# Kernel optimization log

Hardware: AMD Instinct MI355X
Metric: run time of the kernel (lower is better)

Reference implementation:

```python
import jax, jax.numpy as jnp
import numpy as np

B, L, DM, H, DFF = 4, 2048, 512, 8, 2048
D = DM // H            # head dim = 64
FACTOR = 5
U = min(FACTOR * int(np.ceil(np.log(L))), L)  # 40 sampled keys / top-u queries
EPS = 1e-5


def layer_norm(x, g, b):
    m = x.mean(-1, keepdims=True)
    v = ((x - m) ** 2).mean(-1, keepdims=True)
    return (x - m) * jax.lax.rsqrt(v + EPS) * g + b


def setup_inputs() -> dict:
    key = jax.random.key(0)
    ks = jax.random.split(key, 18)
    s = 0.02  # init scale for stability
    return {
        "x": jax.random.normal(ks[0], (B, L, DM), jnp.float32),
        "Wq": jax.random.normal(ks[1], (DM, DM), jnp.float32) * s,
        "bq": jnp.zeros((DM,), jnp.float32),
        "Wk": jax.random.normal(ks[2], (DM, DM), jnp.float32) * s,
        "bk": jnp.zeros((DM,), jnp.float32),
        "Wv": jax.random.normal(ks[3], (DM, DM), jnp.float32) * s,
        "bv": jnp.zeros((DM,), jnp.float32),
        "Wo": jax.random.normal(ks[4], (DM, DM), jnp.float32) * s,
        "bo": jnp.zeros((DM,), jnp.float32),
        "Wc1": jax.random.normal(ks[5], (DFF, DM), jnp.float32) * s,  # conv1d k=1 weight (out,in)
        "bc1": jnp.zeros((DFF,), jnp.float32),
        "Wc2": jax.random.normal(ks[6], (DM, DFF), jnp.float32) * s,
        "bc2": jnp.zeros((DM,), jnp.float32),
        "ln1_g": jnp.ones((DM,), jnp.float32),
        "ln1_b": jnp.zeros((DM,), jnp.float32),
        "ln2_g": jnp.ones((DM,), jnp.float32),
        "ln2_b": jnp.zeros((DM,), jnp.float32),
        "sample_idx": jax.random.randint(ks[7], (L, U), 0, L, jnp.int32),
    }


def reference(x, Wq, bq, Wk, bk, Wv, bv, Wo, bo, Wc1, bc1, Wc2, bc2,
              ln1_g, ln1_b, ln2_g, ln2_b, sample_idx):
    Bb, Ll, _ = x.shape
    # --- AttentionLayer projections -> (B, H, L, D) ---
    q = (x @ Wq + bq).reshape(Bb, Ll, H, D).transpose(0, 2, 1, 3)
    k = (x @ Wk + bk).reshape(Bb, Ll, H, D).transpose(0, 2, 1, 3)
    v = (x @ Wv + bv).reshape(Bb, Ll, H, D).transpose(0, 2, 1, 3)

    # --- ProbSparse: score each query against U sampled keys ---
    K_sample = k[:, :, sample_idx, :]                       # (B,H,L,U,D)
    QK_sample = jnp.einsum('bhld,bhlud->bhlu', q, K_sample)  # (B,H,L,U)
    M = QK_sample.max(-1) - QK_sample.mean(-1)               # sparsity measure (B,H,L)
    _, M_top = jax.lax.top_k(M, U)                           # (B,H,U) top-u query indices

    # --- full attention only for top-u queries ---
    Q_red = jnp.take_along_axis(q, M_top[..., None], axis=2)  # (B,H,U,D)
    scores = jnp.einsum('bhud,bhld->bhul', Q_red, k) / jnp.sqrt(jnp.float32(D))
    attn = jax.nn.softmax(scores, axis=-1)                    # (B,H,U,L)
    ctx_top = jnp.einsum('bhul,bhld->bhud', attn, v)          # (B,H,U,D)

    # --- initial context = mean of V (mask_flag=False); scatter top-u rows ---
    context = jnp.broadcast_to(v.mean(axis=2, keepdims=True), v.shape)
    bi = jnp.arange(Bb)[:, None, None]
    hi = jnp.arange(H)[None, :, None]
    context = context.at[bi, hi, M_top].set(ctx_top)          # (B,H,L,D)

    new_x = context.transpose(0, 2, 1, 3).reshape(Bb, Ll, DM) @ Wo + bo

    # --- residual + norm + conv1d(k=1) FFN + norm ---
    x = layer_norm(x + new_x, ln1_g, ln1_b)
    y = jax.nn.relu(x @ Wc1.T + bc1)
    y = y @ Wc2.T + bc2
    return layer_norm(x + y, ln2_g, ln2_b)
```

## Files before the change

kernel.cpp:

```cpp
#include <hip/hip_runtime.h>
#include <math.h>

static constexpr int Bc = 4, Lc = 2048, DMc = 512, Hc = 8, Dc = 64, DFFc = 2048, Uc = 40;
static constexpr int NT = Bc * Lc;

typedef __attribute__((ext_vector_type(4))) float f32x4;
typedef __attribute__((ext_vector_type(8))) short bf16x8;
typedef unsigned short ushort_t;

__device__ __forceinline__ float wave_sum(float v) {
#pragma unroll
  for (int off = 32; off > 0; off >>= 1) v += __shfl_xor(v, off);
  return v;
}

__device__ __forceinline__ ushort_t f2bf(float f) {
  union { float f; unsigned int u; } c{f};
  unsigned int u = c.u + 0x7fff + ((c.u >> 16) & 1);
  return (ushort_t)(u >> 16);
}

__device__ __forceinline__ float bf2f(ushort_t b) {
  union { unsigned int u; float f; } c{(unsigned int)b << 16};
  return c.f;
}

__device__ __forceinline__ void gload16(const ushort_t* g, ushort_t* l) {
  __builtin_amdgcn_global_load_lds(
      (const __attribute__((address_space(1))) unsigned int*)g,
      (__attribute__((address_space(3))) unsigned int*)l, 16, 0, 0);
}

template <int MODE>
__global__ __launch_bounds__(256) void gemm_mfma(
    const ushort_t* __restrict__ A, const ushort_t* __restrict__ Bt,
    const float* __restrict__ bias, float* __restrict__ Cf,
    ushort_t* __restrict__ Cb, ushort_t* __restrict__ Qo, ushort_t* __restrict__ Ko,
    ushort_t* __restrict__ Vo, int M, int N, int K) {
  __shared__ __align__(16) ushort_t As[128 * 32];
  __shared__ __align__(16) ushort_t Bs[128 * 32];
  const int tid = threadIdx.x;
  const int lane = tid & 63, wave = tid >> 6;
  const int nwg = gridDim.x * gridDim.y;
  const int lin = blockIdx.y * gridDim.x + blockIdx.x;
  const int swz = (lin & 7) * (nwg >> 3) + (lin >> 3);
  const int m0 = (swz / gridDim.x) << 7, n0 = (swz % gridDim.x) << 7;
  const int wm = ((wave >> 1) << 6), wn = ((wave & 1) << 6);
  f32x4 acc[4][4] = {};
  const ushort_t* aSrc = A + (size_t)(m0 + (tid >> 2)) * K + ((tid & 3) << 3);
  const ushort_t* bSrc = Bt + (size_t)(n0 + (tid >> 2)) * K + ((tid & 3) << 3);
  ushort_t* aDst = As + wave * 512;
  ushort_t* bDst = Bs + wave * 512;
  const size_t aHalf = (size_t)64 * K, bHalf = (size_t)64 * K;
  for (int k0 = 0; k0 < K; k0 += 32) {
    gload16(aSrc + k0, aDst);
    gload16(aSrc + aHalf + k0, aDst + 2048);
    gload16(bSrc + k0, bDst);
    gload16(bSrc + bHalf + k0, bDst + 2048);
    __syncthreads();
    bf16x8 af[4], bfr[4];
    const int fr = lane & 15, ko = (lane >> 4) << 3;
#pragma unroll
    for (int i = 0; i < 4; ++i) {
      af[i] = *reinterpret_cast<const bf16x8*>(&As[(wm + i * 16 + fr) * 32 + ko]);
      bfr[i] = *reinterpret_cast<const bf16x8*>(&Bs[(wn + i * 16 + fr) * 32 + ko]);
    }
#pragma unroll
    for (int i = 0; i < 4; ++i)
#pragma unroll
      for (int j = 0; j < 4; ++j)
        acc[i][j] = __builtin_amdgcn_mfma_f32_16x16x32_bf16(af[i], bfr[j], acc[i][j], 0, 0, 0);
    __syncthreads();
  }
  const int cr = (lane >> 4) << 2, cc = lane & 15;
#pragma unroll
  for (int j = 0; j < 4; ++j) {
    const int col = n0 + wn + j * 16 + cc;
    const float bsv = bias[col];
#pragma unroll
    for (int i = 0; i < 4; ++i) {
#pragma unroll
      for (int r = 0; r < 4; ++r) {
        const int row = m0 + wm + i * 16 + cr + r;
        float v = acc[i][j][r] + bsv;
        if (MODE == 0) {
          Cf[(size_t)row * N + col] = v;
        } else if (MODE == 1) {
          Cb[(size_t)row * N + col] = f2bf(fmaxf(v, 0.f));
        } else {
          const int which = col >> 9, h = (col >> 6) & 7, d = col & 63;
          const int b = row >> 11, l = row & (Lc - 1);
          const size_t o = ((size_t)(((b << 3) + h) << 11) + l) * 64 + d;
          ushort_t* dst = which == 0 ? Qo : (which == 1 ? Ko : Vo);
          dst[o] = f2bf(v);
        }
      }
    }
  }
}

__global__ __launch_bounds__(256) void conv_bf16(const float* __restrict__ in,
                                                 ushort_t* __restrict__ out) {
  int i = blockIdx.x * 256 + threadIdx.x;
  float4 v = *reinterpret_cast<const float4*>(&in[(size_t)i * 4]);
  ushort4 o;
  o.x = f2bf(v.x); o.y = f2bf(v.y); o.z = f2bf(v.z); o.w = f2bf(v.w);
  *reinterpret_cast<ushort4*>(&out[(size_t)i * 4]) = o;
}

__global__ __launch_bounds__(256) void tconv(const float* __restrict__ in,
                                             ushort_t* __restrict__ out,
                                             int R, int C, int rowOff) {
  __shared__ float t[32][33];
  const int r0 = blockIdx.y << 5, c0 = blockIdx.x << 5;
  const int tr = threadIdx.x >> 5, tc = threadIdx.x & 31;
#pragma unroll
  for (int p = 0; p < 4; ++p)
    t[tr + p * 8][tc] = in[(size_t)(r0 + tr + p * 8) * C + c0 + tc];
  __syncthreads();
#pragma unroll
  for (int p = 0; p < 4; ++p)
    out[(size_t)(rowOff + c0 + tr + p * 8) * R + r0 + tc] = f2bf(t[tc][tr + p * 8]);
}

__global__ __launch_bounds__(256) void concat_bias(const float* __restrict__ bq,
                                                   const float* __restrict__ bk,
                                                   const float* __restrict__ bv,
                                                   float* __restrict__ o) {
  int i = blockIdx.x * 256 + threadIdx.x;
  o[i] = i < 512 ? bq[i] : (i < 1024 ? bk[i - 512] : bv[i - 1024]);
}

__global__ __launch_bounds__(256) void compute_M_kernel(
    const ushort_t* __restrict__ Q, const ushort_t* __restrict__ K,
    const int* __restrict__ sidx, float* __restrict__ Mout) {
  const int tid = threadIdx.x;
  const int wave = tid >> 6, lane = tid & 63;
  const int g = lane >> 4, lg = lane & 15;
  const int p = blockIdx.x;
  const int xcd = p & 7, j = p >> 3;
  const int bh = xcd + ((j >> 7) << 3);
  const int inner = j & 127;
  const int gw = (bh << 11) + (inner << 4) + wave * 4 + g;
  const int l = gw & (Lc - 1);
  const ushort4 q4 = *reinterpret_cast<const ushort4*>(&Q[((size_t)gw << 6) + (lg << 2)]);
  const float qx = bf2f(q4.x), qy = bf2f(q4.y), qz = bf2f(q4.z), qw = bf2f(q4.w);
  const ushort_t* Kbase = K + ((size_t)bh << 17);
  const int* sp = sidx + l * Uc;
  float mx = -1e30f, sm = 0.f;
#pragma unroll 4
  for (int u = 0; u < Uc; ++u) {
    const int idx = sp[u];
    const ushort4 k4 = *reinterpret_cast<const ushort4*>(&Kbase[((size_t)idx << 6) + (lg << 2)]);
    float d = qx * bf2f(k4.x) + qy * bf2f(k4.y) + qz * bf2f(k4.z) + qw * bf2f(k4.w);
#pragma unroll
    for (int off = 8; off > 0; off >>= 1) d += __shfl_xor(d, off);
    mx = fmaxf(mx, d);
    sm += d;
  }
  if (lg == 0) Mout[gw] = mx - sm * (1.f / Uc);
}

__global__ __launch_bounds__(256) void topk_kernel(const float* __restrict__ Min,
                                                   int* __restrict__ Mtop) {
  __shared__ float sm[Lc];
  const int bh = blockIdx.x >> 3, chunk = blockIdx.x & 7;
  const int tid = threadIdx.x;
  for (int i = tid; i < Lc; i += 256) sm[i] = Min[bh * Lc + i];
  __syncthreads();
  const int cand = (chunk << 8) + tid;
  const float mv = sm[cand];
  int rank = 0;
  for (int j = 0; j < Lc; j += 4) {
    float4 w4 = *reinterpret_cast<const float4*>(&sm[j]);
    rank += (w4.x > mv || (w4.x == mv && (j + 0) < cand));
    rank += (w4.y > mv || (w4.y == mv && (j + 1) < cand));
    rank += (w4.z > mv || (w4.z == mv && (j + 2) < cand));
    rank += (w4.w > mv || (w4.w == mv && (j + 3) < cand));
  }
  if (rank < Uc) Mtop[bh * Uc + rank] = cand;
}

__global__ __launch_bounds__(256, 3) void attn_flash(
    const ushort_t* __restrict__ Q, const ushort_t* __restrict__ K,
    const ushort_t* __restrict__ V, const int* __restrict__ Mtop,
    float* __restrict__ m_p, float* __restrict__ l_p, float* __restrict__ o_p) {
  __shared__ __align__(16) ushort_t Qs[48 * 80];
  __shared__ __align__(16) ushort_t KVs[128 * 80];
  __shared__ __align__(16) ushort_t Ps[48 * 144];
  __shared__ float mw[4][48];
  __shared__ float lw[4][48];
  const int tid = threadIdx.x;
  const int lane = tid & 63, w = tid >> 6;
  const int cc = lane & 15, hi = lane >> 4;
  const int bh = blockIdx.x >> 4, chunk = blockIdx.x & 15;
  const int kk0 = chunk << 7;
  const ushort_t* Qb = Q + ((size_t)bh << 17);
  const ushort_t* Kb = K + ((size_t)bh << 17);
  const ushort_t* Vb = V + ((size_t)bh << 17);

  for (int i = tid; i < 48 * 8; i += 256) {
    const int r = i >> 3, c8 = (i & 7) << 3;
    bf16x8 v = 0;
    if (r < Uc) {
      const int lsel = Mtop[bh * Uc + r];
      v = *reinterpret_cast<const bf16x8*>(&Qb[((size_t)lsel << 6) + c8]);
    }
    *reinterpret_cast<bf16x8*>(&Qs[r * 80 + c8]) = v;
  }
  for (int i = tid; i < 128 * 8; i += 256) {
    const int r = i >> 3, c8 = (i & 7) << 3;
    *reinterpret_cast<bf16x8*>(&KVs[r * 80 + c8]) =
        *reinterpret_cast<const bf16x8*>(&Kb[((size_t)(kk0 + r) << 6) + c8]);
  }
  __syncthreads();

  f32x4 sacc[3][2] = {};
#pragma unroll
  for (int s = 0; s < 2; ++s) {
    bf16x8 af[3], bk[2];
#pragma unroll
    for (int i = 0; i < 3; ++i)
      af[i] = *reinterpret_cast<const bf16x8*>(&Qs[(i * 16 + cc) * 80 + s * 32 + hi * 8]);
#pragma unroll
    for (int jj = 0; jj < 2; ++jj)
      bk[jj] = *reinterpret_cast<const bf16x8*>(&KVs[(w * 32 + jj * 16 + cc) * 80 + s * 32 + hi * 8]);
#pragma unroll
    for (int i = 0; i < 3; ++i)
#pragma unroll
      for (int jj = 0; jj < 2; ++jj)
        sacc[i][jj] = __builtin_amdgcn_mfma_f32_16x16x32_bf16(af[i], bk[jj], sacc[i][jj], 0, 0, 0);
  }

  float mx[3][4];
#pragma unroll
  for (int i = 0; i < 3; ++i)
#pragma unroll
    for (int r = 0; r < 4; ++r)
      mx[i][r] = fmaxf(sacc[i][0][r], sacc[i][1][r]) * 0.125f;
#pragma unroll
  for (int off = 1; off < 16; off <<= 1)
#pragma unroll
    for (int i = 0; i < 3; ++i)
#pragma unroll
      for (int r = 0; r < 4; ++r)
        mx[i][r] = fmaxf(mx[i][r], __shfl_xor(mx[i][r], off));
  if (cc == 0)
#pragma unroll
    for (int i = 0; i < 3; ++i)
#pragma unroll
      for (int r = 0; r < 4; ++r) mw[w][i * 16 + (hi << 2) + r] = mx[i][r];
  __syncthreads();

  float fm[3][4], ls[3][4];
#pragma unroll
  for (int i = 0; i < 3; ++i)
#pragma unroll
    for (int r = 0; r < 4; ++r) {
      const int row = i * 16 + (hi << 2) + r;
      fm[i][r] = fmaxf(fmaxf(mw[0][row], mw[1][row]), fmaxf(mw[2][row], mw[3][row]));
      ls[i][r] = 0.f;
    }
#pragma unroll
  for (int i = 0; i < 3; ++i)
#pragma unroll
    for (int jj = 0; jj < 2; ++jj)
#pragma unroll
      for (int r = 0; r < 4; ++r) {
        float p = __expf(sacc[i][jj][r] * 0.125f - fm[i][r]);
        ls[i][r] += p;
        Ps[(i * 16 + (hi << 2) + r) * 144 + w * 32 + jj * 16 + cc] = f2bf(p);
      }
#pragma unroll
  for (int off = 1; off < 16; off <<= 1)
#pragma unroll
    for (int i = 0; i < 3; ++i)
#pragma unroll
      for (int r = 0; r < 4; ++r) ls[i][r] += __shfl_xor(ls[i][r], off);
  if (cc == 0)
#pragma unroll
    for (int i = 0; i < 3; ++i)
#pragma unroll
      for (int r = 0; r < 4; ++r) lw[w][i * 16 + (hi << 2) + r] = ls[i][r];

  {
    ushort_t* Vt = KVs;
    for (int i = tid; i < 128 * 8; i += 256) {
      const int k = i >> 3, c8 = (i & 7) << 3;
      bf16x8 v = *reinterpret_cast<const bf16x8*>(&Vb[((size_t)(kk0 + k) << 6) + c8]);
#pragma unroll
      for (int jq = 0; jq < 8; ++jq) Vt[(c8 + jq) * 144 + k] = (ushort_t)v[jq];
    }
  }
  __syncthreads();

  f32x4 oacc[3] = {};
#pragma unroll
  for (int s = 0; s < 4; ++s) {
    bf16x8 ap[3], bv;
#pragma unroll
    for (int i = 0; i < 3; ++i)
      ap[i] = *reinterpret_cast<const bf16x8*>(&Ps[(i * 16 + cc) * 144 + s * 32 + hi * 8]);
    bv = *reinterpret_cast<const bf16x8*>(&KVs[(w * 16 + cc) * 144 + s * 32 + hi * 8]);
#pragma unroll
    for (int i = 0; i < 3; ++i)
      oacc[i] = __builtin_amdgcn_mfma_f32_16x16x32_bf16(ap[i], bv, oacc[i], 0, 0, 0);
  }
#pragma unroll
  for (int i = 0; i < 3; ++i)
#pragma unroll
    for (int r = 0; r < 4; ++r) {
      const int row = i * 16 + (hi << 2) + r;
      if (row < Uc)
        o_p[((size_t)((bh * Uc + row) * 16 + chunk) << 6) + w * 16 + cc] = oacc[i][r];
    }
  if (w == 0 && cc == 0)
#pragma unroll
    for (int i = 0; i < 3; ++i)
#pragma unroll
      for (int r = 0; r < 4; ++r) {
        const int row = i * 16 + (hi << 2) + r;
        if (row < Uc) {
          m_p[(bh * Uc + row) * 16 + chunk] = fm[i][r];
          l_p[(bh * Uc + row) * 16 + chunk] =
              lw[0][row] + lw[1][row] + lw[2][row] + lw[3][row];
        }
      }
}

__global__ __launch_bounds__(256) void attn_combine(
    const float* __restrict__ m_p, const float* __restrict__ l_p,
    const float* __restrict__ o_p, const int* __restrict__ Mtop,
    ushort_t* __restrict__ ctxb) {
  const int w = (blockIdx.x * 256 + threadIdx.x) >> 6;
  const int lane = threadIdx.x & 63;
  const float* mp = m_p + w * 16;
  const float* lp = l_p + w * 16;
  float M = -1e30f;
#pragma unroll
  for (int c = 0; c < 16; ++c) M = fmaxf(M, mp[c]);
  float denom = 0.f;
  float wgt[16];
#pragma unroll
  for (int c = 0; c < 16; ++c) {
    wgt[c] = __expf(mp[c] - M);
    denom += lp[c] * wgt[c];
  }
  float acc = 0.f;
#pragma unroll
  for (int c = 0; c < 16; ++c)
    acc += o_p[((size_t)w * 16 + c) * 64 + lane] * wgt[c];
  const int bh = w / Uc;
  const int b = bh >> 3, h = bh & 7;
  const int lsel = Mtop[w];
  ctxb[(size_t)(b * Lc + lsel) * DMc + (h << 6) + lane] = f2bf(acc / denom);
}

__global__ __launch_bounds__(64) void vmean_kernel(const ushort_t* __restrict__ V,
                                                   float* __restrict__ vmean) {
  int blk = blockIdx.x;
  int bh = blk >> 3, c = blk & 7;
  int lane = threadIdx.x;
  float sm = 0.f;
  int lbase = c << 8;
  for (int l = lbase; l < lbase + 256; ++l)
    sm += bf2f(V[((size_t)(bh * Lc + l) << 6) + lane]);
  atomicAdd(&vmean[(bh << 6) + lane], sm * (1.f / Lc));
}

__global__ __launch_bounds__(256) void build_ctx_kernel(const float* __restrict__ vmean,
                                                        ushort_t* __restrict__ ctxb) {
  int idx = blockIdx.x * 256 + threadIdx.x;
  ctxb[idx] = f2bf(vmean[((idx >> 20) << 9) + (idx & 511)]);
}

__global__ __launch_bounds__(256) void add_ln_kernel(
    const float* __restrict__ resid, const float* __restrict__ yin,
    const float* __restrict__ g, const float* __restrict__ bbias,
    float* __restrict__ out, ushort_t* __restrict__ outb) {
  __shared__ float vals[DMc];
  __shared__ float red[4];
  int row = blockIdx.x, tid = threadIdx.x;
  size_t base = (size_t)row * DMc;
  float lsum = 0.f;
  for (int c = tid; c < DMc; c += 256) {
    float t = resid[base + c] + yin[base + c];
    vals[c] = t;
    lsum += t;
  }
  lsum = wave_sum(lsum);
  if ((tid & 63) == 0) red[tid >> 6] = lsum;
  __syncthreads();
  float mean = (red[0] + red[1] + red[2] + red[3]) * (1.f / DMc);
  __syncthreads();
  float lv = 0.f;
  for (int c = tid; c < DMc; c += 256) {
    float dv = vals[c] - mean;
    lv += dv * dv;
  }
  lv = wave_sum(lv);
  if ((tid & 63) == 0) red[tid >> 6] = lv;
  __syncthreads();
  float inv = rsqrtf((red[0] + red[1] + red[2] + red[3]) * (1.f / DMc) + 1e-5f);
  for (int c = tid; c < DMc; c += 256) {
    float o = (vals[c] - mean) * inv * g[c] + bbias[c];
    out[base + c] = o;
    if (outb) outb[base + c] = f2bf(o);
  }
}

extern "C" void kernel_launch(void* const* d_in, const int* in_sizes, int n_in,
                              void* d_out, int out_size, void* d_ws, size_t ws_size,
                              hipStream_t stream) {
  (void)in_sizes; (void)n_in; (void)out_size; (void)ws_size;
  const float* x   = (const float*)d_in[0];
  const float* Wq  = (const float*)d_in[1];
  const float* bq  = (const float*)d_in[2];
  const float* Wk  = (const float*)d_in[3];
  const float* bk  = (const float*)d_in[4];
  const float* Wv  = (const float*)d_in[5];
  const float* bv  = (const float*)d_in[6];
  const float* Wo  = (const float*)d_in[7];
  const float* bo  = (const float*)d_in[8];
  const float* Wc1 = (const float*)d_in[9];
  const float* bc1 = (const float*)d_in[10];
  const float* Wc2 = (const float*)d_in[11];
  const float* bc2 = (const float*)d_in[12];
  const float* g1  = (const float*)d_in[13];
  const float* b1  = (const float*)d_in[14];
  const float* g2  = (const float*)d_in[15];
  const float* b2  = (const float*)d_in[16];
  const int* sidx  = (const int*)d_in[17];
  float* out = (float*)d_out;

  float* ws = (float*)d_ws;
  ushort_t* Qb   = (ushort_t*)ws;
  ushort_t* Kb   = (ushort_t*)(ws + 4194304);
  ushort_t* Vb   = (ushort_t*)(ws + 8388608);
  float* m_p    = ws + 12582912;
  float* l_p    = ws + 12603392;
  float* o_p    = ws + 12623872;
  float* X1     = ws + 16777216;
  ushort_t* xb   = (ushort_t*)(ws + 20971520);
  ushort_t* Wqkvt= (ushort_t*)(ws + 23068672);
  ushort_t* Wot  = (ushort_t*)(ws + 23461888);
  ushort_t* Wc1b = (ushort_t*)(ws + 23592960);
  ushort_t* Wc2b = (ushort_t*)(ws + 24117248);
  float* bqkv   = ws + 24641536;
  float* Mb     = ws + 24643072;
  float* vmean  = ws + 24708608;
  int* Mtop     = (int*)(ws + 24710656);
  ushort_t* CTXb = Vb;
  ushort_t* X1b  = (ushort_t*)(ws + 12582912);
  ushort_t* Yb   = (ushort_t*)ws;

  dim3 blk(256);
  conv_bf16<<<4096, blk, 0, stream>>>(x, xb);
  tconv<<<dim3(16, 16), blk, 0, stream>>>(Wq, Wqkvt, 512, 512, 0);
  tconv<<<dim3(16, 16), blk, 0, stream>>>(Wk, Wqkvt, 512, 512, 512);
  tconv<<<dim3(16, 16), blk, 0, stream>>>(Wv, Wqkvt, 512, 512, 1024);
  tconv<<<dim3(16, 16), blk, 0, stream>>>(Wo, Wot, 512, 512, 0);
  conv_bf16<<<1024, blk, 0, stream>>>(Wc1, Wc1b);
  conv_bf16<<<1024, blk, 0, stream>>>(Wc2, Wc2b);
  concat_bias<<<6, blk, 0, stream>>>(bq, bk, bv, bqkv);

  gemm_mfma<2><<<dim3(12, 64), blk, 0, stream>>>(xb, Wqkvt, bqkv, nullptr, nullptr,
                                                 Qb, Kb, Vb, NT, 1536, DMc);
  compute_M_kernel<<<4096, blk, 0, stream>>>(Qb, Kb, sidx, Mb);
  topk_kernel<<<256, blk, 0, stream>>>(Mb, Mtop);
  attn_flash<<<512, blk, 0, stream>>>(Qb, Kb, Vb, Mtop, m_p, l_p, o_p);
  hipMemsetAsync(vmean, 0, Bc * Hc * Dc * sizeof(float), stream);
  vmean_kernel<<<Bc * Hc * 8, dim3(64), 0, stream>>>(Vb, vmean);
  build_ctx_kernel<<<16384, blk, 0, stream>>>(vmean, CTXb);
  attn_combine<<<320, blk, 0, stream>>>(m_p, l_p, o_p, Mtop, CTXb);

  gemm_mfma<0><<<dim3(4, 64), blk, 0, stream>>>(CTXb, Wot, bo, out, nullptr,
                                                nullptr, nullptr, nullptr,
                                                NT, DMc, DMc);
  add_ln_kernel<<<NT, blk, 0, stream>>>(x, out, g1, b1, X1, X1b);
  gemm_mfma<1><<<dim3(16, 64), blk, 0, stream>>>(X1b, Wc1b, bc1, nullptr, Yb,
                                                 nullptr, nullptr, nullptr,
                                                 NT, DFFc, DMc);
  gemm_mfma<0><<<dim3(4, 64), blk, 0, stream>>>(Yb, Wc2b, bc2, out, nullptr,
                                                nullptr, nullptr, nullptr,
                                                NT, DMc, DFFc);
  add_ln_kernel<<<NT, blk, 0, stream>>>(X1, out, g2, b2, out, nullptr);
}
```

Baseline: 382.0 us.

## Replace brute-force rank top-k with radix bisection threshold and candidate ranking

The top-k kernel changes from ranking all 2048 queries against every other score to one block per (batch, head). Each block maps floats to order-preserving unsigned keys and bisects over the key range with block-wide counts to find the 40th-largest threshold. Only the candidates at or above that threshold are then ranked exactly, with each wave splitting the comparison across its lanes. This removes the O(L^2) comparison work but adds 32 serial bisection rounds, each with two barriers, and launches only 32 blocks, which leaves most of the GPU idle.

Result: faster. 356.8 us (-6.6%).

```diff
diff --git a/kernel.cpp b/kernel.cpp
--- a/kernel.cpp
+++ b/kernel.cpp
@@ -163,22 +163,64 @@
 
 __global__ __launch_bounds__(256) void topk_kernel(const float* __restrict__ Min,
                                                    int* __restrict__ Mtop) {
-  __shared__ float sm[Lc];
-  const int bh = blockIdx.x >> 3, chunk = blockIdx.x & 7;
+  __shared__ unsigned sm[Lc];
+  __shared__ int scount[4];
+  __shared__ int slist[Lc];
+  __shared__ int snum;
+  const int bh = blockIdx.x;
   const int tid = threadIdx.x;
-  for (int i = tid; i < Lc; i += 256) sm[i] = Min[bh * Lc + i];
-  __syncthreads();
-  const int cand = (chunk << 8) + tid;
-  const float mv = sm[cand];
-  int rank = 0;
-  for (int j = 0; j < Lc; j += 4) {
-    float4 w4 = *reinterpret_cast<const float4*>(&sm[j]);
-    rank += (w4.x > mv || (w4.x == mv && (j + 0) < cand));
-    rank += (w4.y > mv || (w4.y == mv && (j + 1) < cand));
-    rank += (w4.z > mv || (w4.z == mv && (j + 2) < cand));
-    rank += (w4.w > mv || (w4.w == mv && (j + 3) < cand));
-  }
-  if (rank < Uc) Mtop[bh * Uc + rank] = cand;
+  const int wv = tid >> 6, lane = tid & 63;
+  unsigned sv[8];
+#pragma unroll
+  for (int t = 0; t < 8; ++t) {
+    const unsigned u = __float_as_uint(Min[bh * Lc + tid + (t << 8)]);
+    const unsigned s = (u & 0x80000000u) ? ~u : (u | 0x80000000u);
+    sv[t] = s;
+    sm[tid + (t << 8)] = s;
+  }
+  if (tid == 0) snum = 0;
+  __syncthreads();
+  unsigned lo = 0u, hi = 0xFFFFFFFFu;
+  while (lo < hi) {
+    const unsigned mid =
+        (unsigned)(((unsigned long long)lo + (unsigned long long)hi + 1ull) >> 1);
+    int cnt = 0;
+#pragma unroll
+    for (int t = 0; t < 8; ++t) cnt += (sv[t] >= mid);
+#pragma unroll
+    for (int off = 32; off > 0; off >>= 1) cnt += __shfl_xor(cnt, off);
+    if (lane == 0) scount[wv] = cnt;
+    __syncthreads();
+    const int total = scount[0] + scount[1] + scount[2] + scount[3];
+    __syncthreads();
+    if (total >= Uc) lo = mid; else hi = mid - 1;
+  }
+#pragma unroll
+  for (int t = 0; t < 8; ++t)
+    if (sv[t] >= lo) {
+      const int pos = atomicAdd(&snum, 1);
+      slist[pos] = tid + (t << 8);
+    }
+  __syncthreads();
+  const int S = snum;
+  const int jbase = lane << 5;
+  for (int s = wv; s < S; s += 4) {
+    const int c = slist[s];
+    const unsigned mv = sm[c];
+    int rank = 0;
+#pragma unroll
+    for (int q = 0; q < 8; ++q) {
+      const int j = jbase + (q << 2);
+      const uint4 w4 = *reinterpret_cast<const uint4*>(&sm[j]);
+      rank += (w4.x > mv || (w4.x == mv && (j + 0) < c));
+      rank += (w4.y > mv || (w4.y == mv && (j + 1) < c));
+      rank += (w4.z > mv || (w4.z == mv && (j + 2) < c));
+      rank += (w4.w > mv || (w4.w == mv && (j + 3) < c));
+    }
+#pragma unroll
+    for (int off = 32; off > 0; off >>= 1) rank += __shfl_xor(rank, off);
+    if (lane == 0 && rank < Uc) Mtop[bh * Uc + rank] = c;
+  }
 }
 
 __global__ __launch_bounds__(256, 3) void attn_flash(
@@ -467,7 +509,7 @@
   gemm_mfma<2><<<dim3(12, 64), blk, 0, stream>>>(xb, Wqkvt, bqkv, nullptr, nullptr,
                                                  Qb, Kb, Vb, NT, 1536, DMc);
   compute_M_kernel<<<4096, blk, 0, stream>>>(Qb, Kb, sidx, Mb);
-  topk_kernel<<<256, blk, 0, stream>>>(Mb, Mtop);
+  topk_kernel<<<32, blk, 0, stream>>>(Mb, Mtop);
   attn_flash<<<512, blk, 0, stream>>>(Qb, Kb, Vb, Mtop, m_p, l_p, o_p);
   hipMemsetAsync(vmean, 0, Bc * Hc * Dc * sizeof(float), stream);
   vmean_kernel<<<Bc * Hc * 8, dim3(64), 0, stream>>>(Vb, vmean);
```
